# Kernel tuning notes

Measured on AMD Instinct MI355X. Metric: run time of the kernel, lower is better.

## Reference

```python
import jax, jax.numpy as jnp
import numpy as np

EPS = 1e-08
TEMPERATURE = 0.05


def setup_inputs() -> dict:
    key = jax.random.key(0)
    k1, k2 = jax.random.split(key)
    N = 8192
    predict_similarity = jax.random.normal(k1, (N,), dtype=jnp.float32)
    true_similarity = jax.random.uniform(k2, (N,), dtype=jnp.float32)
    return {"predict_similarity": predict_similarity, "true_similarity": true_similarity}


def reference(predict_similarity, true_similarity):
    # Sort descending by ground-truth score
    order = jnp.argsort(-true_similarity)
    yt = true_similarity[order]                      # (N,)
    yp = (predict_similarity / TEMPERATURE)[order]   # (N,)
    N = yt.shape[0]

    # Pairwise ground-truth gaps W[k, j] = yt[k] - yt[j]
    W = yt[:, None] - yt[None, :]                    # (N, N)
    # negatives: strictly later in the sorted order AND strictly lower score
    tri = jnp.triu(jnp.ones((N, N), dtype=bool), 1)
    mask = tri & (W > EPS)
    row_valid = jnp.any(mask, axis=1)                # rows contributing to the loss

    neg_inf = jnp.float32(-jnp.inf)
    # weight for the positive = max gap among its valid negatives
    weight_k = jnp.max(jnp.where(mask, W, neg_inf), axis=1)
    weight_k = jnp.where(row_valid, weight_k, 0.0)

    logit_pos = yp * weight_k                        # (N,)
    L_neg = yp[None, :] * W                          # (N, N) negative logits

    # stable masked logsumexp over {pos} U {masked negatives}
    m = jnp.maximum(logit_pos, jnp.max(jnp.where(mask, L_neg, neg_inf), axis=1))
    m = jnp.where(row_valid, m, 0.0)
    z = jnp.where(mask, L_neg - m[:, None], neg_inf)  # exp(-inf)=0 for masked-out
    sum_exp = jnp.exp(logit_pos - m) + jnp.sum(jnp.exp(z), axis=1)
    log_prob = logit_pos - m - jnp.log(sum_exp)      # log_softmax(...)[0]

    count = jnp.sum(row_valid)
    total = jnp.sum(jnp.where(row_valid, log_prob, 0.0))
    return jnp.where(count > 0, -total / jnp.maximum(count, 1).astype(total.dtype), 0.0)
```

## Files before the change

### kernel.cpp

```cpp
#include <hip/hip_runtime.h>
#include <hip/hip_bf16.h>

#define NN 8192
#define NB 8192
#define EPSF 1e-8f
#define LOG2E 1.4426950408889634f
#define LN2f 0.6931471805599453f
#define BLOCK 256
#define CHUNKS 4
#define CH (NN / CHUNKS)
#define RG (NN / 16)
#define A2SCALE (20.0f * LOG2E)

__global__ __launch_bounds__(1024) void sort_kernel(const float* __restrict__ yt,
                                                    const float* __restrict__ pred,
                                                    float* __restrict__ ybkt,
                                                    float* __restrict__ a2bkt,
                                                    int* __restrict__ offs) {
    __shared__ int hist[NB];
    __shared__ int wsum[16], wexcl[16];
    const int t = threadIdx.x, lane = t & 63, wave = t >> 6;

    for (int k = t; k < NB; k += 1024) hist[k] = 0;
    __syncthreads();

    float yv[8]; int bv[8];
#pragma unroll
    for (int k = 0; k < 8; ++k) {
        int i = t + k * 1024;
        float y = yt[i];
        int b = min((int)(y * 8192.0f), NB - 1);
        yv[k] = y; bv[k] = b;
        atomicAdd(&hist[b], 1);
    }
    __syncthreads();

    int local[8]; int sum = 0;
#pragma unroll
    for (int k = 0; k < 8; ++k) { local[k] = hist[t * 8 + k]; sum += local[k]; }
    int incl = sum;
    for (int d = 1; d < 64; d <<= 1) {
        int n = __shfl_up(incl, d);
        if (lane >= d) incl += n;
    }
    if (lane == 63) wsum[wave] = incl;
    __syncthreads();
    if (t < 16) {
        int v = wsum[t], inc2 = v;
        for (int d = 1; d < 16; d <<= 1) {
            int n = __shfl_up(inc2, d);
            if (t >= d) inc2 += n;
        }
        wexcl[t] = inc2 - v;
    }
    __syncthreads();
    int run = wexcl[wave] + incl - sum;
#pragma unroll
    for (int k = 0; k < 8; ++k) {
        hist[t * 8 + k] = run;
        offs[t * 8 + k] = run;
        run += local[k];
    }
    if (t == 1023) offs[NB] = run;
    __syncthreads();

#pragma unroll
    for (int k = 0; k < 8; ++k) {
        int i = t + k * 1024;
        int pos = atomicAdd(&hist[bv[k]], 1);
        ybkt[pos] = yv[k];
        a2bkt[pos] = pred[i] * A2SCALE;
    }
}

__global__ __launch_bounds__(BLOCK) void pro_main(const float* __restrict__ ybkt,
                                                  const float* __restrict__ a2bkt,
                                                  const int* __restrict__ offs,
                                                  float2* __restrict__ partial) {
    const int t = threadIdx.x;
    const int rg = blockIdx.x >> 2;
    const int c  = blockIdx.x & 3;
    const int j0 = c * CH;
    const int wave = t >> 6, lane = t & 63;
    const int row0 = rg * 16 + wave * 4;

    {
        float xl = ybkt[rg * 16 + 15];
        int bl = min((int)(xl * 8192.0f), NB - 1);
        if (offs[bl + 1] <= j0) {
            if (lane == 0) {
#pragma unroll
                for (int r = 0; r < 4; ++r)
                    partial[c * NN + row0 + r] = make_float2(-INFINITY, 0.0f);
            }
            return;
        }
    }

    float x[4], M[4];
#pragma unroll
    for (int r = 0; r < 4; ++r) { x[r] = ybkt[row0 + r]; M[r] = -INFINITY; }
    int u0, end3;
    {
        int b0 = min((int)(x[0] * 8192.0f), NB - 1);
        u0 = (b0 > 0) ? offs[b0 - 1] : 0;
        int b3 = min((int)(x[3] * 8192.0f), NB - 1);
        end3 = offs[b3 + 1];
    }
    int lo = min(max(u0 - j0, 0), CH);
    const int nbi = lo >> 7;
    lo = nbi << 7;
    const int hi = min(max(end3 - j0, lo), CH);
    const int stage_n = min(CH, (hi + 127) & ~127);

    __shared__ float y_s[CH];
    __shared__ float4 ac_s[CH / 2];
    const float4* yb4 = (const float4*)(ybkt + j0);
    const float4* ab4 = (const float4*)(a2bkt + j0);
    float4* ys4 = (float4*)y_s;
    for (int i = t; i < stage_n / 4; i += BLOCK) {
        float4 y4 = yb4[i];
        float4 a4 = ab4[i];
        ys4[i] = y4;
        ac_s[2 * i]     = make_float4(a4.x, a4.x * y4.x, a4.y, a4.y * y4.y);
        ac_s[2 * i + 1] = make_float4(a4.z, a4.z * y4.z, a4.w, a4.w * y4.w);
    }
    __syncthreads();

    for (int i = 0; i < nbi; ++i) {
        float4 v = ac_s[i * 64 + lane];
#pragma unroll
        for (int r = 0; r < 4; ++r) {
            float L0 = __builtin_fmaf(v.x, x[r], -v.y);
            float L1 = __builtin_fmaf(v.z, x[r], -v.w);
            M[r] = fmaxf(M[r], fmaxf(L0, L1));
        }
    }
    for (int base = lo; base < hi; base += 128) {
        int e = base + lane * 2;
        float y0 = y_s[e], y1 = y_s[e + 1];
        float4 v = ac_s[(base >> 1) + lane];
#pragma unroll
        for (int r = 0; r < 4; ++r) {
            float W0 = x[r] - y0, W1 = x[r] - y1;
            float L0 = __builtin_fmaf(v.x, x[r], -v.y);
            float L1 = __builtin_fmaf(v.z, x[r], -v.w);
            L0 = (W0 > EPSF) ? L0 : -INFINITY;
            L1 = (W1 > EPSF) ? L1 : -INFINITY;
            M[r] = fmaxf(M[r], fmaxf(L0, L1));
        }
    }
#pragma unroll
    for (int r = 0; r < 4; ++r)
        for (int m = 1; m < 64; m <<= 1) M[r] = fmaxf(M[r], __shfl_xor(M[r], m));

    float s[4] = {0.f, 0.f, 0.f, 0.f};
    for (int i = 0; i < nbi; ++i) {
        float4 v = ac_s[i * 64 + lane];
#pragma unroll
        for (int r = 0; r < 4; ++r) {
            float t0 = __builtin_fmaf(v.x, x[r], -v.y) - M[r];
            float t1 = __builtin_fmaf(v.z, x[r], -v.w) - M[r];
            s[r] += exp2f(t0) + exp2f(t1);
        }
    }
    for (int base = lo; base < hi; base += 128) {
        int e = base + lane * 2;
        float y0 = y_s[e], y1 = y_s[e + 1];
        float4 v = ac_s[(base >> 1) + lane];
#pragma unroll
        for (int r = 0; r < 4; ++r) {
            float W0 = x[r] - y0, W1 = x[r] - y1;
            float t0 = __builtin_fmaf(v.x, x[r], -v.y) - M[r];
            float t1 = __builtin_fmaf(v.z, x[r], -v.w) - M[r];
            t0 = (W0 > EPSF) ? t0 : -INFINITY;
            t1 = (W1 > EPSF) ? t1 : -INFINITY;
            s[r] += exp2f(t0) + exp2f(t1);
        }
    }
#pragma unroll
    for (int r = 0; r < 4; ++r)
        for (int m = 1; m < 64; m <<= 1) s[r] += __shfl_xor(s[r], m);

    if (lane == 0) {
#pragma unroll
        for (int r = 0; r < 4; ++r)
            partial[c * NN + row0 + r] = make_float2(M[r], s[r]);
    }
}

__global__ __launch_bounds__(1024) void finalize(const float* __restrict__ ybkt,
                                                 const float* __restrict__ a2bkt,
                                                 const float2* __restrict__ partial,
                                                 float* __restrict__ out) {
    __shared__ float redm[16];
    __shared__ float2 red2[16];
    __shared__ float bmin;
    const int t = threadIdx.x, lane = t & 63, wave = t >> 6;

    float mn = INFINITY;
    for (int i = t; i < NN; i += 1024) mn = fminf(mn, ybkt[i]);
#pragma unroll
    for (int m = 1; m < 64; m <<= 1) mn = fminf(mn, __shfl_xor(mn, m));
    if (lane == 0) redm[wave] = mn;
    __syncthreads();
    if (t == 0) {
        float v = redm[0];
        for (int i = 1; i < 16; ++i) v = fminf(v, redm[i]);
        bmin = v;
    }
    __syncthreads();
    const float yt_min = bmin;

    float wtot = 0.f, wcnt = 0.f;
    for (int p = t; p < NN; p += 1024) {
        float x = ybkt[p];
        float w = x - yt_min;
        float lp = a2bkt[p] * w;
        float2 pc[CHUNKS];
        float M = lp;
#pragma unroll
        for (int c = 0; c < CHUNKS; ++c) {
            pc[c] = partial[c * NN + p];
            M = fmaxf(M, pc[c].x);
        }
        float sum = exp2f(lp - M);
#pragma unroll
        for (int c = 0; c < CHUNKS; ++c) sum += pc[c].y * exp2f(pc[c].x - M);
        float logp = (lp - M) * LN2f - __logf(sum);
        if (w > EPSF) { wtot += logp; wcnt += 1.f; }
    }
#pragma unroll
    for (int m = 1; m < 64; m <<= 1) { wtot += __shfl_xor(wtot, m); wcnt += __shfl_xor(wcnt, m); }
    if (lane == 0) red2[wave] = make_float2(wtot, wcnt);
    __syncthreads();
    if (t == 0) {
        float bt = 0.f, bc = 0.f;
        for (int i = 0; i < 16; ++i) { bt += red2[i].x; bc += red2[i].y; }
        out[0] = (bc > 0.f) ? (-bt / bc) : 0.f;
    }
}

extern "C" void kernel_launch(void* const* d_in, const int* in_sizes, int n_in,
                              void* d_out, int out_size, void* d_ws, size_t ws_size,
                              hipStream_t stream) {
    const float* pred = (const float*)d_in[0];
    const float* yt   = (const float*)d_in[1];

    float* ybkt  = (float*)d_ws;
    float* a2bkt = ybkt + NN;
    int*   offs  = (int*)(a2bkt + NN);
    float2* partial = (float2*)(offs + NN + 2);

    sort_kernel<<<1, 1024, 0, stream>>>(yt, pred, ybkt, a2bkt, offs);
    pro_main<<<RG * CHUNKS, BLOCK, 0, stream>>>(ybkt, a2bkt, offs, partial);
    finalize<<<1, 1024, 0, stream>>>(ybkt, a2bkt, partial, (float*)d_out);
}
```

Before: 98.83 us.

## Split single-block bucket sort into multi-block histogram, scan and scatter kernels

Replaces the one-block counting sort with three kernels: a grid-wide histogram built with global atomics, a single-block prefix scan, and a grid-wide scatter that uses global atomic cursors. A memset clears the histogram first. The aim is to spread the histogram and scatter work over many CUs instead of serialising 8192 elements on one block. In exchange it adds three extra launches or dispatches and uses global rather than LDS atomics, which may cost more than the single-block kernel took.

```diff
diff --git a/kernel.cpp b/kernel.cpp
--- a/kernel.cpp
+++ b/kernel.cpp
@@ -12,28 +12,19 @@
 #define RG (NN / 16)
 #define A2SCALE (20.0f * LOG2E)
 
-__global__ __launch_bounds__(1024) void sort_kernel(const float* __restrict__ yt,
-                                                    const float* __restrict__ pred,
-                                                    float* __restrict__ ybkt,
-                                                    float* __restrict__ a2bkt,
-                                                    int* __restrict__ offs) {
-    __shared__ int hist[NB];
+__global__ __launch_bounds__(256) void khist(const float* __restrict__ yt,
+                                             int* __restrict__ hist) {
+    int i = blockIdx.x * 256 + threadIdx.x;
+    float y = yt[i];
+    int b = min(max((int)(y * 8192.0f), 0), NB - 1);
+    atomicAdd(&hist[b], 1);
+}
+
+__global__ __launch_bounds__(1024) void kscan(const int* __restrict__ hist,
+                                              int* __restrict__ offs,
+                                              int* __restrict__ cursor) {
     __shared__ int wsum[16], wexcl[16];
     const int t = threadIdx.x, lane = t & 63, wave = t >> 6;
-
-    for (int k = t; k < NB; k += 1024) hist[k] = 0;
-    __syncthreads();
-
-    float yv[8]; int bv[8];
-#pragma unroll
-    for (int k = 0; k < 8; ++k) {
-        int i = t + k * 1024;
-        float y = yt[i];
-        int b = min((int)(y * 8192.0f), NB - 1);
-        yv[k] = y; bv[k] = b;
-        atomicAdd(&hist[b], 1);
-    }
-    __syncthreads();
 
     int local[8]; int sum = 0;
 #pragma unroll
@@ -57,20 +48,24 @@
     int run = wexcl[wave] + incl - sum;
 #pragma unroll
     for (int k = 0; k < 8; ++k) {
-        hist[t * 8 + k] = run;
         offs[t * 8 + k] = run;
+        cursor[t * 8 + k] = run;
         run += local[k];
     }
     if (t == 1023) offs[NB] = run;
-    __syncthreads();
-
-#pragma unroll
-    for (int k = 0; k < 8; ++k) {
-        int i = t + k * 1024;
-        int pos = atomicAdd(&hist[bv[k]], 1);
-        ybkt[pos] = yv[k];
-        a2bkt[pos] = pred[i] * A2SCALE;
-    }
+}
+
+__global__ __launch_bounds__(256) void kscatter(const float* __restrict__ yt,
+                                                const float* __restrict__ pred,
+                                                int* __restrict__ cursor,
+                                                float* __restrict__ ybkt,
+                                                float* __restrict__ a2bkt) {
+    int i = blockIdx.x * 256 + threadIdx.x;
+    float y = yt[i];
+    int b = min(max((int)(y * 8192.0f), 0), NB - 1);
+    int pos = atomicAdd(&cursor[b], 1);
+    ybkt[pos] = y;
+    a2bkt[pos] = pred[i] * A2SCALE;
 }
 
 __global__ __launch_bounds__(BLOCK) void pro_main(const float* __restrict__ ybkt,
@@ -247,12 +242,17 @@
     const float* pred = (const float*)d_in[0];
     const float* yt   = (const float*)d_in[1];
 
-    float* ybkt  = (float*)d_ws;
-    float* a2bkt = ybkt + NN;
-    int*   offs  = (int*)(a2bkt + NN);
-    float2* partial = (float2*)(offs + NN + 2);
-
-    sort_kernel<<<1, 1024, 0, stream>>>(yt, pred, ybkt, a2bkt, offs);
+    float* ybkt   = (float*)d_ws;
+    float* a2bkt  = ybkt + NN;
+    int*   offs   = (int*)(a2bkt + NN);
+    int*   hist   = offs + NN + 2;
+    int*   cursor = hist + NB;
+    float2* partial = (float2*)(cursor + NB);
+
+    hipMemsetAsync(hist, 0, NB * sizeof(int), stream);
+    khist<<<NN / 256, 256, 0, stream>>>(yt, hist);
+    kscan<<<1, 1024, 0, stream>>>(hist, offs, cursor);
+    kscatter<<<NN / 256, 256, 0, stream>>>(yt, pred, cursor, ybkt, a2bkt);
     pro_main<<<RG * CHUNKS, BLOCK, 0, stream>>>(ybkt, a2bkt, offs, partial);
     finalize<<<1, 1024, 0, stream>>>(ybkt, a2bkt, partial, (float*)d_out);
 }
```

Result: faster. 95.52 us (-3.4%).
